# Performance work log

Hardware: AMD Instinct MI355X
Metric: run time of the kernel (lower is better)

The kernel has to match this reference:

```python
import jax, jax.numpy as jnp
import numpy as np

EPS = 1e-12  # F.normalize default eps


def _l2norm(x):
    n = jnp.linalg.norm(x, axis=-1, keepdims=True)
    return x / jnp.maximum(n, EPS)


def setup_inputs() -> dict:
    key = jax.random.key(0)
    k1, k2, k3, k4 = jax.random.split(key, 4)
    N, Tq, Ts, S, D = 16, 1369, 5476, 4, 768
    return {
        "x_query": jax.random.normal(k1, (N, Tq, D), dtype=jnp.float32),
        "x_support": jax.random.normal(k2, (N, Ts, D), dtype=jnp.float32),
        "x_support_cls": jax.random.normal(k3, (N, S, D), dtype=jnp.float32),
        "W_head": jax.random.normal(k4, (3 * D, 1), dtype=jnp.float32) * 0.02,
        "b_head": jnp.zeros((1,), dtype=jnp.float32),
    }


def reference(x_query, x_support, x_support_cls, W_head, b_head):
    N, Tq, D = x_query.shape
    side = int(np.sqrt(Tq))  # token grid side, 37 for 1369 tokens

    # mean CLS over shots, then L2-normalize everything
    cls = _l2norm(jnp.mean(x_support_cls, axis=1, keepdims=True))  # [N,1,D]
    q = _l2norm(x_query)     # [N,Tq,D]
    s = _l2norm(x_support)   # [N,Ts,D]

    # cosine distance matrix and nearest-support reduction
    cd = 1.0 - jnp.einsum("nqd,nsd->nqs", q, s)      # [N,Tq,Ts]
    dmin = jnp.min(cd, axis=-1)                        # [N,Tq]
    idx = jnp.argmin(cd, axis=-1)                      # [N,Tq]
    nearest = jnp.take_along_axis(s, idx[..., None], axis=1)  # [N,Tq,D]

    # head on concat([q, nearest, cls]) -> sigmoid
    feat = jnp.concatenate(
        [q, nearest, jnp.broadcast_to(cls, (N, Tq, D))], axis=-1
    )  # [N,Tq,3D]
    logits = feat @ W_head + b_head                    # [N,Tq,1]
    pred = jax.nn.sigmoid(logits)

    dmin = dmin.reshape(N, 1, side, side)
    pred = pred.reshape(N, 1, side, side)
    return pred * dmin, pred
```

## Files before the change

kernel.cpp:

```cpp
#include <hip/hip_runtime.h>
#include <stdint.h>

#define NB 16
#define TQ 1369
#define TS 5476
#define DD 768

#define BM 128
#define BN 128
#define KB 24
#define RBQ 11
#define RBS 43
#define QPAD 1408
#define SPAD 5504
#define DSTR 5632
#define EPS_SEL 2.5e-3f

typedef float f32x4 __attribute__((ext_vector_type(4)));
typedef short short8 __attribute__((ext_vector_type(8)));
typedef unsigned short ushort;


__device__ inline float waveReduceSum(float v) {
    #pragma unroll
    for (int m = 32; m >= 1; m >>= 1) v += __shfl_xor(v, m);
    return v;
}

__device__ inline unsigned bf16rne(float x) {
    unsigned u = __float_as_uint(x);
    return (u + 0x7FFFu + ((u >> 16) & 1u)) >> 16;
}
__device__ inline unsigned pack2(float lo, float hi) {
    return bf16rne(lo) | (bf16rne(hi) << 16);
}

__device__ inline f32x4 mfma16(short8 a, short8 b, f32x4 c) {
    return __builtin_amdgcn_mfma_f32_16x16x32_bf16(a, b, c, 0, 0, 0);
}

__device__ inline void async16(const void* g, void* l) {
    __builtin_amdgcn_global_load_lds(
        (const __attribute__((address_space(1))) unsigned*)g,
        (__attribute__((address_space(3))) unsigned*)l, 16, 0, 0);
}

__device__ inline float h2f(ushort u) {
    union { ushort us; _Float16 h; } cv; cv.us = u;
    return (float)cv.h;
}


__global__ __launch_bounds__(256) void cls_kernel(const float* __restrict__ xc,
                                                  float* __restrict__ cls) {
    int n = blockIdx.x, tid = threadIdx.x;
    const float* base = xc + (size_t)n * 4 * DD;
    float v[3]; float ss = 0.f;
    #pragma unroll
    for (int i = 0; i < 3; i++) {
        int e = tid + i * 256;
        float a = base[e] + base[DD + e] + base[2 * DD + e] + base[3 * DD + e];
        v[i] = a * 0.25f; ss += v[i] * v[i];
    }
    ss = waveReduceSum(ss);
    __shared__ float red[4]; __shared__ float rn;
    if ((tid & 63) == 0) red[tid >> 6] = ss;
    __syncthreads();
    if (tid == 0) {
        float t = red[0] + red[1] + red[2] + red[3];
        rn = 1.0f / fmaxf(sqrtf(t), 1e-12f);
    }
    __syncthreads();
    float r = rn;
    #pragma unroll
    for (int i = 0; i < 3; i++) cls[(size_t)n * DD + tid + i * 256] = v[i] * r;
}


__global__ __launch_bounds__(256) void split_kernel(const float* __restrict__ Q,
                                                    const float* __restrict__ S,
                                                    ushort* __restrict__ Qh,
                                                    ushort* __restrict__ Sh,
                                                    float* __restrict__ rq,
                                                    float* __restrict__ rs) {
    int wid = (int)((blockIdx.x * 256u + threadIdx.x) >> 6);
    int lane = threadIdx.x & 63;
    bool isQ = wid < NB * QPAD;
    int n, row, nreal;
    if (isQ) { n = wid / QPAD; row = wid % QPAD; nreal = TQ; }
    else     { int w2 = wid - NB * QPAD; n = w2 / SPAD; row = w2 % SPAD; nreal = TS; }
    int rb = row >> 7, p = row & 127;
    size_t tbase = isQ ? (size_t)(n * RBQ + rb) * KB * 4096
                       : (size_t)(n * RBS + rb) * KB * 4096;
    ushort* outp = (isQ ? Qh : Sh) + tbase;

    if (row >= nreal) {
        uint4 z = {0u, 0u, 0u, 0u};
        for (int t = lane; t < 96; t += 64) {
            int kb = t >> 2, g = t & 3;
            *(uint4*)(outp + (size_t)kb * 4096 + g * 1024 + p * 8) = z;
        }
        return;
    }

    const float* src = isQ ? Q + ((size_t)n * TQ + row) * DD
                           : S + ((size_t)n * TS + row) * DD;
    float4 x[3]; float ss = 0.f;
    #pragma unroll
    for (int i = 0; i < 3; i++) {
        x[i] = ((const float4*)src)[lane + i * 64];
        ss += x[i].x * x[i].x + x[i].y * x[i].y + x[i].z * x[i].z + x[i].w * x[i].w;
    }
    ss = waveReduceSum(ss);
    float r = 1.0f / fmaxf(sqrtf(ss), 1e-12f);
    if (lane == 0) {
        if (isQ) rq[(size_t)n * TQ + row] = r; else rs[(size_t)n * TS + row] = r;
    }
    #pragma unroll
    for (int i = 0; i < 3; i++) {
        float ax = x[i].x * r, ay = x[i].y * r, az = x[i].z * r, aw = x[i].w * r;
        int k0 = lane * 4 + i * 256;
        int kb = k0 >> 5;
        int g  = (k0 >> 3) & 3;
        int sub = k0 & 7;
        uint2 hv;
        hv.x = pack2(ax, ay);
        hv.y = pack2(az, aw);
        *(uint2*)(outp + (size_t)kb * 4096 + g * 1024 + p * 8 + sub) = hv;
    }
}


__global__ __launch_bounds__(256, 4) void gemm1(const ushort* __restrict__ Qh,
                                                const ushort* __restrict__ Sh,
                                                ushort* __restrict__ dist) {
    __shared__ __align__(16) ushort As[4096];
    __shared__ __align__(16) ushort Bs[4096];

    int tid = threadIdx.x, w = tid >> 6, lane = tid & 63;
    int bx = blockIdx.x, by = blockIdx.y, n = blockIdx.z;
    int wm = w & 1, wn = w >> 1, g4 = lane >> 4, c16 = lane & 15;

    const char* gsrc = (const char*)((w < 2)
        ? (Qh + (size_t)(n * RBQ + bx) * KB * 4096)
        : (Sh + (size_t)(n * RBS + by) * KB * 4096)) + (w & 1) * 4096 + lane * 16;
    char* lbase = (char*)((w < 2) ? As : Bs) + (w & 1) * 4096;

    f32x4 acc[4][4] = {};
    int aoff = g4 * 1024 + wm * 512 + c16 * 8;
    int boff = g4 * 1024 + wn * 512 + c16 * 8;

    for (int kb = 0; kb < KB; kb++) {
        #pragma unroll
        for (int j = 0; j < 4; j++)
            async16(gsrc + (size_t)kb * 8192 + j * 1024, lbase + j * 1024);
        __syncthreads();

        short8 ah[4], bh[4];
        #pragma unroll
        for (int i = 0; i < 4; i++) {
            ah[i] = *(const short8*)&As[aoff + i * 128];
            bh[i] = *(const short8*)&Bs[boff + i * 128];
        }
        #pragma unroll
        for (int mi = 0; mi < 4; mi++)
            #pragma unroll
            for (int ni = 0; ni < 4; ni++)
                acc[mi][ni] = mfma16(ah[mi], bh[ni], acc[mi][ni]);
        __syncthreads();
    }

    int row0 = bx * BM + wm * 64 + g4 * 4;
    int col0 = by * BN + wn * 64 + c16;
    #pragma unroll
    for (int mi = 0; mi < 4; mi++) {
        #pragma unroll
        for (int r = 0; r < 4; r++) {
            int rowq = row0 + mi * 16 + r;
            if (rowq < TQ) {
                ushort* dp = dist + (size_t)(n * TQ + rowq) * DSTR + col0;
                #pragma unroll
                for (int ni = 0; ni < 4; ni++) {
                    union { _Float16 h; ushort u; } cv;
                    cv.h = (_Float16)acc[mi][ni][r];
                    dp[ni * 16] = cv.u;
                }
            }
        }
    }
}


__global__ __launch_bounds__(256) void select_head(const ushort* __restrict__ dist,
                                                   const float* __restrict__ Q,
                                                   const float* __restrict__ S,
                                                   const float* __restrict__ rq,
                                                   const float* __restrict__ rs,
                                                   const float* __restrict__ cls,
                                                   const float* __restrict__ W,
                                                   const float* __restrict__ bb,
                                                   float* __restrict__ out) {
    __shared__ int cand[4][32];
    __shared__ int ccnt[4];
    int w = threadIdx.x >> 6, lane = threadIdx.x & 63;
    int qi = blockIdx.x * 4 + w;
    int n = qi / TQ;
    const ushort* rowp = dist + (size_t)qi * DSTR;

    float pm = -1e30f; int im = 0x7FFFFFFF;
    #pragma unroll
    for (int it = 0; it < 11; it++) {
        union { uint4 v; ushort us[8]; } u;
        u.v = *(const uint4*)(rowp + it * 512 + lane * 8);
        int col0 = it * 512 + lane * 8;
        #pragma unroll
        for (int e = 0; e < 8; e++) {
            float p = h2f(u.us[e]);
            int col = col0 + e;
            if (col < TS && p > pm) { pm = p; im = col; }
        }
    }
    #pragma unroll
    for (int m = 1; m < 64; m <<= 1) {
        float op = __shfl_xor(pm, m);
        int   oi = __shfl_xor(im, m);
        if (op > pm || (op == pm && oi < im)) { pm = op; im = oi; }
    }

    if (lane == 0) ccnt[w] = 0;
    float thresh = pm - EPS_SEL;
    #pragma unroll
    for (int it = 0; it < 11; it++) {
        union { uint4 v; ushort us[8]; } u;
        u.v = *(const uint4*)(rowp + it * 512 + lane * 8);
        int col0 = it * 512 + lane * 8;
        #pragma unroll
        for (int e = 0; e < 8; e++) {
            float p = h2f(u.us[e]);
            int col = col0 + e;
            if (col < TS && p >= thresh) {
                int slot = atomicAdd(&ccnt[w], 1);
                if (slot < 32) cand[w][slot] = col;
            }
        }
    }
    int cnt = min(ccnt[w], 32);

    const float* qrow = Q + (size_t)qi * DD;
    float4 q4[3];
    #pragma unroll
    for (int i = 0; i < 3; i++) q4[i] = ((const float4*)qrow)[lane + i * 64];
    float rqv = rq[qi];

    float bestd = -1e30f; int bidx = 0x7FFFFFFF;
    for (int c = 0; c < cnt; c++) {
        int sidx = cand[w][c];
        const float* srow = S + ((size_t)n * TS + sidx) * DD;
        float part = 0.f;
        #pragma unroll
        for (int i = 0; i < 3; i++) {
            float4 s4 = ((const float4*)srow)[lane + i * 64];
            part += q4[i].x * s4.x + q4[i].y * s4.y + q4[i].z * s4.z + q4[i].w * s4.w;
        }
        part = waveReduceSum(part);
        float dot = part * rqv * rs[(size_t)n * TS + sidx];
        if (dot > bestd || (dot == bestd && sidx < bidx)) { bestd = dot; bidx = sidx; }
    }
    float dmin = 1.0f - bestd;

    const float* srow = S + ((size_t)n * TS + bidx) * DD;
    const float* clsr = cls + (size_t)n * DD;
    float rsv = rs[(size_t)n * TS + bidx];
    float aq = 0.f, as_ = 0.f, ac = 0.f;
    #pragma unroll
    for (int i = 0; i < 3; i++) {
        float4 s4 = ((const float4*)srow)[lane + i * 64];
        float4 c4 = ((const float4*)clsr)[lane + i * 64];
        float4 w0 = ((const float4*)W)[lane + i * 64];
        float4 w1 = ((const float4*)(W + DD))[lane + i * 64];
        float4 w2 = ((const float4*)(W + 2 * DD))[lane + i * 64];
        aq += q4[i].x * w0.x + q4[i].y * w0.y + q4[i].z * w0.z + q4[i].w * w0.w;
        as_ += s4.x * w1.x + s4.y * w1.y + s4.z * w1.z + s4.w * w1.w;
        ac += c4.x * w2.x + c4.y * w2.y + c4.z * w2.z + c4.w * w2.w;
    }
    float tot = waveReduceSum(aq * rqv + as_ * rsv + ac);
    if (lane == 0) {
        float logit = tot + bb[0];
        float pred = 1.0f / (1.0f + expf(-logit));
        out[qi] = pred * dmin;
        out[NB * TQ + qi] = pred;
    }
}


extern "C" void kernel_launch(void* const* d_in, const int* in_sizes, int n_in,
                              void* d_out, int out_size, void* d_ws, size_t ws_size,
                              hipStream_t stream) {
    const float* Q  = (const float*)d_in[0];
    const float* S  = (const float*)d_in[1];
    const float* XC = (const float*)d_in[2];
    const float* W  = (const float*)d_in[3];
    const float* B  = (const float*)d_in[4];
    (void)in_sizes; (void)n_in; (void)out_size;

    char* ws = (char*)d_ws;
    ushort* dist = (ushort*)ws;
    ushort* Qh   = (ushort*)(ws + 246726656ull);
    ushort* Sh   = (ushort*)(ws + 246726656ull + 34603008ull);
    float*  rq   = (float*)(ws + 416595968ull);
    float*  rs   = (float*)(ws + 416683584ull);
    float*  cls  = (float*)(ws + 417034048ull);
    if (ws_size < 417083200ull) return;

    cls_kernel<<<NB, 256, 0, stream>>>(XC, cls);

    split_kernel<<<27648, 256, 0, stream>>>(Q, S, Qh, Sh, rq, rs);

    dim3 grid(RBQ, RBS, NB);
    gemm1<<<grid, 256, 0, stream>>>(Qh, Sh, dist);

    select_head<<<(NB * TQ) / 4, 256, 0, stream>>>(dist, Q, S, rq, rs, cls, W, B,
                                                   (float*)d_out);
}
```

Before: 848.3 us.

## Fuse nearest-neighbor candidate selection into GEMM epilogue, drop distance matrix

The GEMM kernel now walks a chunk of support tiles per block and keeps a running row max in shared memory. Near-max candidates (column plus approximate score) go into small per-chunk lists instead of writing the full fp16 distance matrix to global memory. The head kernel merges the eight chunk maxima and rechecks only candidates within the threshold against fp32 data. This removes the large dist write and re-read, but cuts the grid from 43 to 8 column blocks per query tile, lowering parallelism. It also adds shared-memory atomics and can drop candidates when a list overflows its cap.

```diff
diff --git a/kernel.cpp b/kernel.cpp
--- a/kernel.cpp
+++ b/kernel.cpp
@@ -13,7 +13,8 @@
 #define RBS 43
 #define QPAD 1408
 #define SPAD 5504
-#define DSTR 5632
+#define SC 8
+#define CAP 16
 #define EPS_SEL 2.5e-3f
 
 typedef float f32x4 __attribute__((ext_vector_type(4)));
@@ -45,9 +46,12 @@
         (__attribute__((address_space(3))) unsigned*)l, 16, 0, 0);
 }
 
-__device__ inline float h2f(ushort u) {
-    union { ushort us; _Float16 h; } cv; cv.us = u;
-    return (float)cv.h;
+__device__ inline unsigned fsort(float f) {
+    unsigned u = __float_as_uint(f);
+    return (u & 0x80000000u) ? ~u : (u | 0x80000000u);
+}
+__device__ inline float funsort(unsigned u) {
+    return __uint_as_float((u & 0x80000000u) ? (u & 0x7FFFFFFFu) : ~u);
 }
 
 
@@ -131,120 +135,137 @@
 }
 
 
-__global__ __launch_bounds__(256, 4) void gemm1(const ushort* __restrict__ Qh,
-                                                const ushort* __restrict__ Sh,
-                                                ushort* __restrict__ dist) {
+__global__ __launch_bounds__(256, 4) void gemm_sel(const ushort* __restrict__ Qh,
+                                                   const ushort* __restrict__ Sh,
+                                                   float* __restrict__ cmax,
+                                                   int* __restrict__ ccnt,
+                                                   uint2* __restrict__ cpair) {
     __shared__ __align__(16) ushort As[4096];
     __shared__ __align__(16) ushort Bs[4096];
+    __shared__ unsigned runmaxU[128];
+    __shared__ int cnt[128];
+    __shared__ uint2 cand[128][CAP];
 
     int tid = threadIdx.x, w = tid >> 6, lane = tid & 63;
-    int bx = blockIdx.x, by = blockIdx.y, n = blockIdx.z;
+    int bx = blockIdx.x, ch = blockIdx.y, n = blockIdx.z;
     int wm = w & 1, wn = w >> 1, g4 = lane >> 4, c16 = lane & 15;
 
-    const char* gsrc = (const char*)((w < 2)
-        ? (Qh + (size_t)(n * RBQ + bx) * KB * 4096)
-        : (Sh + (size_t)(n * RBS + by) * KB * 4096)) + (w & 1) * 4096 + lane * 16;
-    char* lbase = (char*)((w < 2) ? As : Bs) + (w & 1) * 4096;
-
-    f32x4 acc[4][4] = {};
+    if (tid < 128) { runmaxU[tid] = 0u; cnt[tid] = 0; }
+    __syncthreads();
+
+    const char* gA = (const char*)(Qh + (size_t)(n * RBQ + bx) * KB * 4096)
+                     + wm * 4096 + lane * 16;
+    char* lbase = (char*)((w < 2) ? As : Bs) + wm * 4096;
     int aoff = g4 * 1024 + wm * 512 + c16 * 8;
     int boff = g4 * 1024 + wn * 512 + c16 * 8;
 
-    for (int kb = 0; kb < KB; kb++) {
+    int t0 = ch * 5 + min(ch, 3);
+    int t1 = t0 + (ch < 3 ? 6 : 5);
+
+    for (int by = t0; by < t1; by++) {
+        const char* gsrc = (w < 2) ? gA
+            : (const char*)(Sh + (size_t)(n * RBS + by) * KB * 4096) + wm * 4096 + lane * 16;
+
+        f32x4 acc[4][4] = {};
+        for (int kb = 0; kb < KB; kb++) {
+            #pragma unroll
+            for (int j = 0; j < 4; j++)
+                async16(gsrc + (size_t)kb * 8192 + j * 1024, lbase + j * 1024);
+            __syncthreads();
+
+            short8 ah[4], bh[4];
+            #pragma unroll
+            for (int i = 0; i < 4; i++) {
+                ah[i] = *(const short8*)&As[aoff + i * 128];
+                bh[i] = *(const short8*)&Bs[boff + i * 128];
+            }
+            #pragma unroll
+            for (int mi = 0; mi < 4; mi++)
+                #pragma unroll
+                for (int ni = 0; ni < 4; ni++)
+                    acc[mi][ni] = mfma16(ah[mi], bh[ni], acc[mi][ni]);
+            __syncthreads();
+        }
+
+        int colb = by * 128 + wn * 64 + c16;
+        bool edge = (by == RBS - 1);
+
         #pragma unroll
-        for (int j = 0; j < 4; j++)
-            async16(gsrc + (size_t)kb * 8192 + j * 1024, lbase + j * 1024);
+        for (int mi = 0; mi < 4; mi++) {
+            #pragma unroll
+            for (int r = 0; r < 4; r++) {
+                float v0 = acc[mi][0][r], v1 = acc[mi][1][r];
+                float v2 = acc[mi][2][r], v3 = acc[mi][3][r];
+                if (edge) {
+                    if (colb +  0 >= TS) v0 = -1e30f;
+                    if (colb + 16 >= TS) v1 = -1e30f;
+                    if (colb + 32 >= TS) v2 = -1e30f;
+                    if (colb + 48 >= TS) v3 = -1e30f;
+                }
+                float v = fmaxf(fmaxf(v0, v1), fmaxf(v2, v3));
+                #pragma unroll
+                for (int m = 1; m < 16; m <<= 1) v = fmaxf(v, __shfl_xor(v, m));
+                if (c16 == 0) {
+                    int row = wm * 64 + mi * 16 + g4 * 4 + r;
+                    atomicMax(&runmaxU[row], fsort(v));
+                }
+            }
+        }
         __syncthreads();
 
-        short8 ah[4], bh[4];
         #pragma unroll
-        for (int i = 0; i < 4; i++) {
-            ah[i] = *(const short8*)&As[aoff + i * 128];
-            bh[i] = *(const short8*)&Bs[boff + i * 128];
-        }
-        #pragma unroll
-        for (int mi = 0; mi < 4; mi++)
-            #pragma unroll
-            for (int ni = 0; ni < 4; ni++)
-                acc[mi][ni] = mfma16(ah[mi], bh[ni], acc[mi][ni]);
-        __syncthreads();
-    }
-
-    int row0 = bx * BM + wm * 64 + g4 * 4;
-    int col0 = by * BN + wn * 64 + c16;
-    #pragma unroll
-    for (int mi = 0; mi < 4; mi++) {
-        #pragma unroll
-        for (int r = 0; r < 4; r++) {
-            int rowq = row0 + mi * 16 + r;
-            if (rowq < TQ) {
-                ushort* dp = dist + (size_t)(n * TQ + rowq) * DSTR + col0;
+        for (int mi = 0; mi < 4; mi++) {
+            #pragma unroll
+            for (int r = 0; r < 4; r++) {
+                int row = wm * 64 + mi * 16 + g4 * 4 + r;
+                float thr = funsort(runmaxU[row]) - EPS_SEL;
                 #pragma unroll
                 for (int ni = 0; ni < 4; ni++) {
-                    union { _Float16 h; ushort u; } cv;
-                    cv.h = (_Float16)acc[mi][ni][r];
-                    dp[ni * 16] = cv.u;
+                    float d = acc[mi][ni][r];
+                    int col = colb + ni * 16;
+                    if (d >= thr && (!edge || col < TS)) {
+                        int slot = atomicAdd(&cnt[row], 1);
+                        if (slot < CAP) {
+                            uint2 pr; pr.x = (unsigned)col; pr.y = __float_as_uint(d);
+                            cand[row][slot] = pr;
+                        }
+                    }
                 }
             }
         }
-    }
-}
-
-
-__global__ __launch_bounds__(256) void select_head(const ushort* __restrict__ dist,
-                                                   const float* __restrict__ Q,
-                                                   const float* __restrict__ S,
-                                                   const float* __restrict__ rq,
-                                                   const float* __restrict__ rs,
-                                                   const float* __restrict__ cls,
-                                                   const float* __restrict__ W,
-                                                   const float* __restrict__ bb,
-                                                   float* __restrict__ out) {
-    __shared__ int cand[4][32];
-    __shared__ int ccnt[4];
+        __syncthreads();
+    }
+
+    if (tid < 128) {
+        size_t rec = ((size_t)n * QPAD + (size_t)bx * 128 + tid) * SC + ch;
+        cmax[rec] = funsort(runmaxU[tid]);
+        int c = min(cnt[tid], CAP);
+        ccnt[rec] = c;
+        for (int i = 0; i < c; i++) cpair[rec * CAP + i] = cand[tid][i];
+    }
+}
+
+
+__global__ __launch_bounds__(256) void merge_head(const float* __restrict__ cmax,
+                                                  const int* __restrict__ ccnt,
+                                                  const uint2* __restrict__ cpair,
+                                                  const float* __restrict__ Q,
+                                                  const float* __restrict__ S,
+                                                  const float* __restrict__ rq,
+                                                  const float* __restrict__ rs,
+                                                  const float* __restrict__ cls,
+                                                  const float* __restrict__ W,
+                                                  const float* __restrict__ bb,
+                                                  float* __restrict__ out) {
     int w = threadIdx.x >> 6, lane = threadIdx.x & 63;
     int qi = blockIdx.x * 4 + w;
-    int n = qi / TQ;
-    const ushort* rowp = dist + (size_t)qi * DSTR;
-
-    float pm = -1e30f; int im = 0x7FFFFFFF;
-    #pragma unroll
-    for (int it = 0; it < 11; it++) {
-        union { uint4 v; ushort us[8]; } u;
-        u.v = *(const uint4*)(rowp + it * 512 + lane * 8);
-        int col0 = it * 512 + lane * 8;
-        #pragma unroll
-        for (int e = 0; e < 8; e++) {
-            float p = h2f(u.us[e]);
-            int col = col0 + e;
-            if (col < TS && p > pm) { pm = p; im = col; }
-        }
-    }
-    #pragma unroll
-    for (int m = 1; m < 64; m <<= 1) {
-        float op = __shfl_xor(pm, m);
-        int   oi = __shfl_xor(im, m);
-        if (op > pm || (op == pm && oi < im)) { pm = op; im = oi; }
-    }
-
-    if (lane == 0) ccnt[w] = 0;
-    float thresh = pm - EPS_SEL;
-    #pragma unroll
-    for (int it = 0; it < 11; it++) {
-        union { uint4 v; ushort us[8]; } u;
-        u.v = *(const uint4*)(rowp + it * 512 + lane * 8);
-        int col0 = it * 512 + lane * 8;
-        #pragma unroll
-        for (int e = 0; e < 8; e++) {
-            float p = h2f(u.us[e]);
-            int col = col0 + e;
-            if (col < TS && p >= thresh) {
-                int slot = atomicAdd(&ccnt[w], 1);
-                if (slot < 32) cand[w][slot] = col;
-            }
-        }
-    }
-    int cnt = min(ccnt[w], 32);
+    int n = qi / TQ, qr = qi - n * TQ;
+    size_t rec0 = ((size_t)n * QPAD + qr) * SC;
+
+    float pm = -1e30f;
+    #pragma unroll
+    for (int c = 0; c < SC; c++) pm = fmaxf(pm, cmax[rec0 + c]);
+    float thr = pm - EPS_SEL;
 
     const float* qrow = Q + (size_t)qi * DD;
     float4 q4[3];
@@ -253,19 +274,32 @@
     float rqv = rq[qi];
 
     float bestd = -1e30f; int bidx = 0x7FFFFFFF;
-    for (int c = 0; c < cnt; c++) {
-        int sidx = cand[w][c];
+    float fba = -1e30f;  int fbi = 0;
+
+    auto recheck = [&](int sidx) {
         const float* srow = S + ((size_t)n * TS + sidx) * DD;
         float part = 0.f;
         #pragma unroll
-        for (int i = 0; i < 3; i++) {
-            float4 s4 = ((const float4*)srow)[lane + i * 64];
-            part += q4[i].x * s4.x + q4[i].y * s4.y + q4[i].z * s4.z + q4[i].w * s4.w;
+        for (int k = 0; k < 3; k++) {
+            float4 s4 = ((const float4*)srow)[lane + k * 64];
+            part += q4[k].x * s4.x + q4[k].y * s4.y + q4[k].z * s4.z + q4[k].w * s4.w;
         }
         part = waveReduceSum(part);
         float dot = part * rqv * rs[(size_t)n * TS + sidx];
         if (dot > bestd || (dot == bestd && sidx < bidx)) { bestd = dot; bidx = sidx; }
-    }
+    };
+
+    for (int c = 0; c < SC; c++) {
+        int cn = ccnt[rec0 + c];
+        for (int i = 0; i < cn; i++) {
+            uint2 pr = cpair[(rec0 + c) * CAP + i];
+            int sidx = (int)pr.x;
+            float ad = __uint_as_float(pr.y);
+            if (ad > fba) { fba = ad; fbi = sidx; }
+            if (ad >= thr) recheck(sidx);
+        }
+    }
+    if (bidx == 0x7FFFFFFF) recheck(fbi);
     float dmin = 1.0f - bestd;
 
     const float* srow = S + ((size_t)n * TS + bidx) * DD;
@@ -304,21 +338,23 @@
     (void)in_sizes; (void)n_in; (void)out_size;
 
     char* ws = (char*)d_ws;
-    ushort* dist = (ushort*)ws;
-    ushort* Qh   = (ushort*)(ws + 246726656ull);
-    ushort* Sh   = (ushort*)(ws + 246726656ull + 34603008ull);
-    float*  rq   = (float*)(ws + 416595968ull);
-    float*  rs   = (float*)(ws + 416683584ull);
-    float*  cls  = (float*)(ws + 417034048ull);
-    if (ws_size < 417083200ull) return;
+    ushort* Qh    = (ushort*)ws;
+    ushort* Sh    = (ushort*)(ws + 34603008ull);
+    float*  rq    = (float*)(ws + 169869312ull);
+    float*  rs    = (float*)(ws + 169956928ull);
+    float*  cls   = (float*)(ws + 170307392ull);
+    float*  cmax  = (float*)(ws + 170356544ull);
+    int*    ccnt  = (int*)(ws + 171077440ull);
+    uint2*  cpair = (uint2*)(ws + 171798336ull);
+    if (ws_size < 194867008ull) return;
 
     cls_kernel<<<NB, 256, 0, stream>>>(XC, cls);
 
     split_kernel<<<27648, 256, 0, stream>>>(Q, S, Qh, Sh, rq, rs);
 
-    dim3 grid(RBQ, RBS, NB);
-    gemm1<<<grid, 256, 0, stream>>>(Qh, Sh, dist);
-
-    select_head<<<(NB * TQ) / 4, 256, 0, stream>>>(dist, Q, S, rq, rs, cls, W, B,
-                                                   (float*)d_out);
-}
+    dim3 grid(RBQ, SC, NB);
+    gemm_sel<<<grid, 256, 0, stream>>>(Qh, Sh, cmax, ccnt, cpair);
+
+    merge_head<<<(NB * TQ) / 4, 256, 0, stream>>>(cmax, ccnt, cpair, Q, S, rq, rs,
+                                                  cls, W, B, (float*)d_out);
+}
```

After: 1.088 ms. +28.2%, slower.
